# Kernel tuning notes

Hardware: AMD Instinct MI355X
Metric: run time of the kernel (lower is better)

## Reference

```python
import jax, jax.numpy as jnp
import numpy as np

N, E, G = 50000, 400000, 2048
H, C = 4, 64            # heads, hidden per head
IN, ED, TASKS = 29, 6, 12
HC = H * C


def setup_inputs() -> dict:
    key = jax.random.key(0)
    ks = jax.random.split(key, 20)
    s = 0.1
    f32 = jnp.float32
    inp = {
        'x': jax.random.normal(ks[0], (N, IN), f32),
        'edge_index': jax.random.randint(ks[1], (2, E), 0, N),
        'edge_attr': jax.random.normal(ks[2], (E, ED), f32),
        'batch': jnp.sort(jax.random.randint(ks[3], (N,), 0, G)),
        # layer 1 (in=29 -> H*C=256)
        'W1': jax.random.normal(ks[4], (IN, HC), f32) * s,
        'as1': jax.random.normal(ks[5], (1, H, C), f32) * s,
        'ad1': jax.random.normal(ks[6], (1, H, C), f32) * s,
        'We1': jax.random.normal(ks[7], (ED, HC), f32) * s,
        'ae1': jax.random.normal(ks[8], (1, H, C), f32) * s,
        'b1': jnp.zeros((HC,), f32),
        # layer 2 (in=256 -> 256)
        'W2': jax.random.normal(ks[9], (HC, HC), f32) * s,
        'as2': jax.random.normal(ks[10], (1, H, C), f32) * s,
        'ad2': jax.random.normal(ks[11], (1, H, C), f32) * s,
        'We2': jax.random.normal(ks[12], (ED, HC), f32) * s,
        'ae2': jax.random.normal(ks[13], (1, H, C), f32) * s,
        'b2': jnp.zeros((HC,), f32),
        # readout linear (256 -> 12)
        'Wl': jax.random.normal(ks[14], (HC, TASKS), f32) * s,
        'bl': jnp.zeros((TASKS,), f32),
    }
    return inp


def _gat_conv(x, src, dst, eattr, W, a_src, a_dst, We, a_e, b):
    """PyG GATConv, concat=True, leaky_relu slope 0.2, self-loops already appended."""
    h = (x @ W).reshape(N, H, C)                      # [N,H,C]
    al_s = jnp.sum(h * a_src, axis=-1)                # [N,H]
    al_d = jnp.sum(h * a_dst, axis=-1)                # [N,H]
    he = (eattr @ We).reshape(-1, H, C)               # [Etot,H,C]
    al_e = jnp.sum(he * a_e, axis=-1)                 # [Etot,H]
    alpha = al_s[src] + al_d[dst] + al_e              # [Etot,H]
    alpha = jax.nn.leaky_relu(alpha, negative_slope=0.2)
    # segment softmax over incoming edges of each dst node
    amax = jax.ops.segment_max(alpha, dst, num_segments=N)
    ex = jnp.exp(alpha - amax[dst])
    denom = jax.ops.segment_sum(ex, dst, num_segments=N)
    alpha = ex / (denom[dst] + 1e-16)
    msg = h[src] * alpha[:, :, None]                  # [Etot,H,C]
    out = jax.ops.segment_sum(msg, dst, num_segments=N)
    return out.reshape(N, HC) + b


def reference(x, edge_index, edge_attr, batch,
              W1, as1, ad1, We1, ae1, b1,
              W2, as2, ad2, We2, ae2, b2, Wl, bl):
    # add self-loops with edge_attr fill = mean over existing edges (PyG default)
    loop = jnp.arange(N)
    src = jnp.concatenate([edge_index[0], loop])
    dst = jnp.concatenate([edge_index[1], loop])
    mean_e = jnp.mean(edge_attr, axis=0, keepdims=True)
    eattr = jnp.concatenate([edge_attr, jnp.broadcast_to(mean_e, (N, ED))], axis=0)

    h = _gat_conv(x, src, dst, eattr, W1, as1, ad1, We1, ae1, b1)
    h = jax.nn.relu(h)
    h = _gat_conv(h, src, dst, eattr, W2, as2, ad2, We2, ae2, b2)
    h = jax.nn.relu(h)

    # global mean pool over graphs
    sums = jax.ops.segment_sum(h, batch, num_segments=G)      # [G,HC]
    cnt = jax.ops.segment_sum(jnp.ones((N,), h.dtype), batch, num_segments=G)
    pooled = sums / jnp.maximum(cnt, 1.0)[:, None]
    return pooled @ Wl + bl
```

## Files before the change

kernel.cpp:

```cpp
#include <hip/hip_runtime.h>
#include <math.h>

static constexpr int NN = 50000;
static constexpr int EE = 400000;
static constexpr int GG = 2048;
static constexpr int TASKS = 12;

typedef __attribute__((ext_vector_type(8))) short short8;
typedef __attribute__((ext_vector_type(4))) float floatx4;

__device__ __forceinline__ unsigned short f2bf(float f) {
  unsigned u = __float_as_uint(f);
  u = u + 0x7fffu + ((u >> 16) & 1u);
  return (unsigned short)(u >> 16);
}
__device__ __forceinline__ float bflo(unsigned u) { return __uint_as_float(u << 16); }
__device__ __forceinline__ float bfhi(unsigned u) { return __uint_as_float(u & 0xffff0000u); }

static constexpr int NBDEG = (EE + 255) / 256;
static constexpr int NBMEAN = 256;
static constexpr int NBX = (NN * 4 + 255) / 256;
static constexpr int NW1 = 32;
static constexpr int NW2 = 256;
__global__ void k_pre(const int* __restrict__ dst, const float* __restrict__ ea,
                      const float* __restrict__ x, const float* __restrict__ W1,
                      const float* __restrict__ W2, int* __restrict__ deg,
                      float* __restrict__ msum, unsigned short* __restrict__ xb,
                      unsigned short* __restrict__ w1t, unsigned short* __restrict__ w2t) {
  const int b = blockIdx.x;
  const int t = threadIdx.x;
  if (b < NBDEG) {
    int e = b * 256 + t;
    if (e < EE) atomicAdd(&deg[dst[e]], 1);
  } else if (b < NBDEG + NBMEAN) {
    float s[6] = {0, 0, 0, 0, 0, 0};
    for (int e = (b - NBDEG) * 256 + t; e < EE; e += NBMEAN * 256) {
#pragma unroll
      for (int d = 0; d < 6; d++) s[d] += ea[(size_t)e * 6 + d];
    }
    __shared__ float ls[6];
    if (t < 6) ls[t] = 0.f;
    __syncthreads();
#pragma unroll
    for (int d = 0; d < 6; d++) atomicAdd(&ls[d], s[d]);
    __syncthreads();
    if (t < 6) atomicAdd(&msum[t], ls[t]);
  } else if (b < NBDEG + NBMEAN + NBX) {
    int i = (b - NBDEG - NBMEAN) * 256 + t;
    if (i < NN * 4) {
      int n = i >> 2, seg = i & 3;
      unsigned short v[8];
#pragma unroll
      for (int j = 0; j < 8; j++) {
        int k = seg * 8 + j;
        v[j] = (k < 29) ? f2bf(x[(size_t)n * 29 + k]) : (unsigned short)0;
      }
      *(short8*)(xb + (size_t)n * 32 + seg * 8) = *(short8*)v;
    }
  } else if (b < NBDEG + NBMEAN + NBX + NW1) {
    int i = (b - NBDEG - NBMEAN - NBX) * 256 + t;
    int row = i >> 5, k = i & 31;
    unsigned short v = (k < 29) ? f2bf(W1[(size_t)k * 256 + row]) : (unsigned short)0;
    w1t[((row >> 4) * 4 + (k >> 3)) * 128 + (row & 15) * 8 + (k & 7)] = v;
  } else {
    int i = (b - NBDEG - NBMEAN - NBX - NW1) * 256 + t;
    int row = i >> 8, k = i & 255;
    w2t[((row >> 4) * 32 + (k >> 3)) * 128 + (row & 15) * 8 + (k & 7)] = f2bf(W2[(size_t)k * 256 + row]);
  }
}

static constexpr int NBS = (NN + 255) / 256;

__global__ void k_scan1(const int* __restrict__ deg, int* __restrict__ rowptr,
                        int* __restrict__ bsums, const float* __restrict__ We1,
                        const float* __restrict__ ae1, const float* __restrict__ We2,
                        const float* __restrict__ ae2, const float* __restrict__ msum,
                        float* __restrict__ p1, float* __restrict__ p2) {
  const int t = threadIdx.x;
  if (blockIdx.x >= NBS) {
    const int layer = blockIdx.x - NBS;
    const float* We = layer ? We2 : We1;
    const float* ae = layer ? ae2 : ae1;
    float* params = layer ? p2 : p1;
    __shared__ float vsh[24];
    if (t < 24) {
      int d = t >> 2, h = t & 3;
      float s = 0.f;
      for (int c = 0; c < 64; c++) s += We[d * 256 + h * 64 + c] * ae[h * 64 + c];
      vsh[t] = s;
      params[t] = s;
    }
    __syncthreads();
    if (t < 4) {
      float s = 0.f;
      const float invE = 1.0f / (float)EE;
#pragma unroll
      for (int d = 0; d < 6; d++) s += (msum[d] * invE) * vsh[d * 4 + t];
      params[24 + t] = s;
    }
    return;
  }
  __shared__ int sh[256];
  int i = blockIdx.x * 256 + t;
  int v = (i < NN) ? deg[i] : 0;
  sh[t] = v;
  __syncthreads();
  for (int off = 1; off < 256; off <<= 1) {
    int tv = (t >= off) ? sh[t - off] : 0;
    __syncthreads();
    sh[t] += tv;
    __syncthreads();
  }
  if (i < NN) rowptr[i] = sh[t] - v;
  if (t == 255) bsums[blockIdx.x] = sh[255];
}

__global__ void k_scan23(int* __restrict__ rowptr, const int* __restrict__ bsums, int nb) {
  __shared__ int sh[256];
  const int t = threadIdx.x;
  sh[t] = (t < nb) ? bsums[t] : 0;
  __syncthreads();
  for (int off = 1; off < 256; off <<= 1) {
    int tv = (t >= off) ? sh[t - off] : 0;
    __syncthreads();
    sh[t] += tv;
    __syncthreads();
  }
  const int add = (blockIdx.x == 0) ? 0 : sh[blockIdx.x - 1];
  int i = blockIdx.x * 256 + t;
  if (i < NN) rowptr[i] += add;
  if (i == 0) rowptr[NN] = EE;
}

template <int KP>
__device__ __forceinline__ void gemm_body(
    int bx, const unsigned short* __restrict__ A, const unsigned short* __restrict__ Bt,
    const float* __restrict__ a_s, const float* __restrict__ a_d,
    unsigned short* __restrict__ Y, float* __restrict__ als, float* __restrict__ ald, int M) {
  __shared__ __align__(16) unsigned short Ash[64 * KP];
  const int tid = threadIdx.x;
  const int lane = tid & 63;
  const int w = tid >> 6;
  const int l15 = lane & 15;
  const int quad = lane >> 4;
  const int row0 = bx * 64;

  constexpr int STEPS = (64 * KP * 2) / (256 * 16);
  {
    const char* Ab = (const char*)(A + (size_t)row0 * KP);
    uint4 stg[STEPS];
#pragma unroll
    for (int s = 0; s < STEPS; s++) stg[s] = *(const uint4*)(Ab + s * 4096 + tid * 16);
#pragma unroll
    for (int s = 0; s < STEPS; s++) {
      int o = s * 4096 + tid * 16;
      int row = o / (KP * 2);
      *(uint4*)((char*)Ash + (o ^ ((row & 7) << 4))) = stg[s];
    }
  }

  floatx4 acc[4][4];
#pragma unroll
  for (int i = 0; i < 4; i++)
#pragma unroll
    for (int j = 0; j < 4; j++) acc[i][j] = {0.f, 0.f, 0.f, 0.f};

  const unsigned short* pb[4];
#pragma unroll
  for (int j = 0; j < 4; j++)
    pb[j] = Bt + (size_t)((w * 4 + j) * (KP / 8) + quad) * 128 + l15 * 8;

  constexpr int NPH = KP / 32;
  short8 bfr[3][4];
#pragma unroll
  for (int j = 0; j < 4; j++) bfr[0][j] = *(const short8*)pb[j];
  if (NPH > 1) {
#pragma unroll
    for (int j = 0; j < 4; j++) {
      pb[j] += 512;
      bfr[1][j] = *(const short8*)pb[j];
    }
  }

  __syncthreads();

  auto ldA = [&](int ph, short8 (&dst)[4]) {
#pragma unroll
    for (int i = 0; i < 4; i++) {
      int lin = (i * 16 + l15) * (KP * 2) + ph * 64 + quad * 16;
      dst[i] = *(const short8*)((const char*)Ash + (lin ^ ((l15 & 7) << 4)));
    }
  };
  short8 af[2][4];
  ldA(0, af[0]);

#pragma unroll
  for (int ph = 0; ph < NPH; ph++) {
    if (ph + 2 < NPH) {
#pragma unroll
      for (int j = 0; j < 4; j++) {
        pb[j] += 512;
        bfr[(ph + 2) % 3][j] = *(const short8*)pb[j];
      }
    }
    if (ph + 1 < NPH) ldA(ph + 1, af[(ph + 1) & 1]);
#pragma unroll
    for (int i = 0; i < 4; i++)
#pragma unroll
      for (int j = 0; j < 4; j++)
        acc[i][j] = __builtin_amdgcn_mfma_f32_16x16x32_bf16(af[ph & 1][i], bfr[ph % 3][j], acc[i][j], 0, 0, 0);
  }
  float asc[4], adc[4];
#pragma unroll
  for (int j = 0; j < 4; j++) {
    asc[j] = a_s[w * 64 + j * 16 + l15];
    adc[j] = a_d[w * 64 + j * 16 + l15];
  }
#pragma unroll
  for (int i = 0; i < 4; i++) {
#pragma unroll
    for (int r = 0; r < 4; r++) {
      const int row = row0 + i * 16 + quad * 4 + r;
      unsigned ub[4];
      float hv[4];
#pragma unroll
      for (int j = 0; j < 4; j++) {
        ub[j] = f2bf(acc[i][j][r]);
        hv[j] = __uint_as_float(ub[j] << 16);
      }
      if (row < M) {
#pragma unroll
        for (int j = 0; j < 4; j++) Y[(size_t)row * 256 + w * 64 + j * 16 + l15] = (unsigned short)ub[j];
      }
      float ps = hv[0] * asc[0] + hv[1] * asc[1] + hv[2] * asc[2] + hv[3] * asc[3];
      float pd = hv[0] * adc[0] + hv[1] * adc[1] + hv[2] * adc[2] + hv[3] * adc[3];
#pragma unroll
      for (int off = 1; off < 16; off <<= 1) {
        ps += __shfl_xor(ps, off, 64);
        pd += __shfl_xor(pd, off, 64);
      }
      if (l15 == 0 && row < M) {
        als[row * 4 + w] = ps;
        ald[row * 4 + w] = pd;
      }
    }
  }
}

static constexpr int GB = (NN + 63) / 64;

__global__ __launch_bounds__(256, 2) void k_scatgemm1(
    const int* __restrict__ ei, const int* __restrict__ rowptr, int* __restrict__ cursor,
    int2* __restrict__ cse,
    const unsigned short* __restrict__ xb, const unsigned short* __restrict__ w1t,
    const float* __restrict__ as1, const float* __restrict__ ad1,
    unsigned short* __restrict__ hb, float* __restrict__ als, float* __restrict__ ald) {
  const int b = blockIdx.x;
  const int t = threadIdx.x;
  if (b < NBDEG) {
    int e = b * 256 + t;
    if (e >= EE) return;
    int s = ei[e];
    int d = ei[EE + e];
    int p = atomicAdd(&cursor[d], 1);
    int slot = rowptr[d] + p;
    cse[slot] = make_int2(s, e);
  } else {
    gemm_body<32>(b - NBDEG, xb, w1t, as1, ad1, hb, als, ald, NN);
  }
}

__global__ __launch_bounds__(256, 2) void k_gemm2(
    const unsigned short* __restrict__ A, const unsigned short* __restrict__ Bt,
    const float* __restrict__ a_s, const float* __restrict__ a_d,
    unsigned short* __restrict__ Y, float* __restrict__ als, float* __restrict__ ald) {
  gemm_body<256>(blockIdx.x, A, Bt, a_s, a_d, Y, als, ald, NN);
}

__global__ void k_edc(const int2* __restrict__ cse, const float* __restrict__ ea,
                      const float* __restrict__ p1, const float* __restrict__ p2,
                      float* __restrict__ ed1, float* __restrict__ ed2) {
  int slot = blockIdx.x * 256 + threadIdx.x;
  if (slot >= EE) return;
  int e = cse[slot].y;
  const float* ep = ea + (size_t)e * 6;
  float2 e0 = *(const float2*)ep;
  float2 e1 = *(const float2*)(ep + 2);
  float2 e2 = *(const float2*)(ep + 4);
  float c1[4], c2[4];
#pragma unroll
  for (int h = 0; h < 4; h++) {
    c1[h] = e0.x * p1[0 * 4 + h] + e0.y * p1[1 * 4 + h] + e1.x * p1[2 * 4 + h] +
            e1.y * p1[3 * 4 + h] + e2.x * p1[4 * 4 + h] + e2.y * p1[5 * 4 + h];
    c2[h] = e0.x * p2[0 * 4 + h] + e0.y * p2[1 * 4 + h] + e1.x * p2[2 * 4 + h] +
            e1.y * p2[3 * 4 + h] + e2.x * p2[4 * 4 + h] + e2.y * p2[5 * 4 + h];
  }
  *(float4*)(ed1 + (size_t)slot * 4) = make_float4(c1[0], c1[1], c1[2], c1[3]);
  *(float4*)(ed2 + (size_t)slot * 4) = make_float4(c2[0], c2[1], c2[2], c2[3]);
}

__device__ __forceinline__ float leaky02(float x) { return x > 0.f ? x : 0.2f * x; }

__global__ __launch_bounds__(256) void k_agg(
    const unsigned short* __restrict__ hinb, const float* __restrict__ als,
    const float* __restrict__ ald, const int* __restrict__ rowptr, const int2* __restrict__ cse,
    const float* __restrict__ edc, const float* __restrict__ params, const float* __restrict__ bias,
    unsigned short* __restrict__ houtb) {
  const int lane = threadIdx.x & 63;
  const int n = blockIdx.x * 4 + (threadIdx.x >> 6);
  if (n >= NN) return;
  const int half = lane >> 5;
  const int sl = lane & 31;
  const int head = sl >> 3;

  const float aldn = ald[n * 4 + head];
  float acc[8];
  float ssum;
  {
    float slg = leaky02(als[n * 4 + head] + aldn + params[24 + head]);
    float exs = __expf(slg);
    float wgt = (half == 0) ? exs : 0.f;
    ssum = wgt;
    uint4 uv = *(const uint4*)(hinb + (size_t)n * 256 + sl * 8);
    acc[0] = bflo(uv.x) * wgt;
    acc[1] = bfhi(uv.x) * wgt;
    acc[2] = bflo(uv.y) * wgt;
    acc[3] = bfhi(uv.y) * wgt;
    acc[4] = bflo(uv.z) * wgt;
    acc[5] = bfhi(uv.z) * wgt;
    acc[6] = bflo(uv.w) * wgt;
    acc[7] = bfhi(uv.w) * wgt;
  }
  const int end = rowptr[n + 1];
  int s = rowptr[n] + half;
  while (s < end) {
    int sid[4];
    float edv[4];
#pragma unroll
    for (int k = 0; k < 4; k++) {
      const int q = s + 2 * k;
      const bool v = q < end;
      const int idx = v ? q : end - 1;
      sid[k] = cse[idx].x;
      edv[k] = v ? edc[(size_t)idx * 4 + head] : 0.f;
    }
    float alv[4];
#pragma unroll
    for (int k = 0; k < 4; k++) alv[k] = als[(size_t)sid[k] * 4 + head];
    uint4 r[4];
#pragma unroll
    for (int k = 0; k < 4; k++) {
      r[k] = make_uint4(0u, 0u, 0u, 0u);
      if (s + 2 * k < end) r[k] = *(const uint4*)(hinb + (size_t)sid[k] * 256 + sl * 8);
    }
#pragma unroll
    for (int k = 0; k < 4; k++) {
      const float ex = (s + 2 * k < end) ? __expf(leaky02(alv[k] + aldn + edv[k])) : 0.f;
      acc[0] += bflo(r[k].x) * ex;
      acc[1] += bfhi(r[k].x) * ex;
      acc[2] += bflo(r[k].y) * ex;
      acc[3] += bfhi(r[k].y) * ex;
      acc[4] += bflo(r[k].z) * ex;
      acc[5] += bfhi(r[k].z) * ex;
      acc[6] += bflo(r[k].w) * ex;
      acc[7] += bfhi(r[k].w) * ex;
      ssum += ex;
    }
    s += 8;
  }
#pragma unroll
  for (int j = 0; j < 8; j++) acc[j] += __shfl_xor(acc[j], 32, 64);
  ssum += __shfl_xor(ssum, 32, 64);
  if (half == 0) {
    const float inv = 1.f / (ssum + 1e-16f);
    float4 b0 = *(const float4*)(bias + sl * 8);
    float4 b1 = *(const float4*)(bias + sl * 8 + 4);
    const float bb[8] = {b0.x, b0.y, b0.z, b0.w, b1.x, b1.y, b1.z, b1.w};
    uint p[4];
#pragma unroll
    for (int j = 0; j < 4; j++) {
      float e0 = fmaxf(acc[2 * j] * inv + bb[2 * j], 0.f);
      float e1 = fmaxf(acc[2 * j + 1] * inv + bb[2 * j + 1], 0.f);
      p[j] = (uint)f2bf(e0) | ((uint)f2bf(e1) << 16);
    }
    *(uint4*)(houtb + (size_t)n * 256 + sl * 8) = make_uint4(p[0], p[1], p[2], p[3]);
  }
}

__global__ __launch_bounds__(256) void k_pool(const unsigned short* __restrict__ hb,
                                              const int* __restrict__ batch,
                                              const float* __restrict__ Wl,
                                              const float* __restrict__ bl,
                                              float* __restrict__ out) {
  int g = blockIdx.x;
  int t = threadIdx.x;
  int lo = 0, hi = NN;
  while (lo < hi) {
    int mid = (lo + hi) >> 1;
    if (batch[mid] < g) lo = mid + 1; else hi = mid;
  }
  int start = lo;
  hi = NN;
  while (lo < hi) {
    int mid = (lo + hi) >> 1;
    if (batch[mid] < g + 1) lo = mid + 1; else hi = mid;
  }
  int end = lo;
  const int mid2 = start + ((end - start) >> 1);
  __shared__ float sp[256], sq[256];
  {
    const int c = t & 127;
    const int hseg = t >> 7;
    const int a = hseg ? mid2 : start;
    const int b = hseg ? end : mid2;
    float s0 = 0.f, s1 = 0.f;
    for (int n2 = a; n2 < b; n2++) {
      uint u = ((const uint*)(hb + (size_t)n2 * 256))[c];
      s0 += bflo(u);
      s1 += bfhi(u);
    }
    float* dst = hseg ? sq : sp;
    dst[2 * c] = s0;
    dst[2 * c + 1] = s1;
  }
  __syncthreads();
  if (t < TASKS) {
    float invc = 1.f / fmaxf((float)(end - start), 1.f);
    float o = bl[t];
    for (int c = 0; c < 256; c++) o += (sp[c] + sq[c]) * invc * Wl[c * 12 + t];
    out[(size_t)g * 12 + t] = o;
  }
}

extern "C" void kernel_launch(void* const* d_in, const int* in_sizes, int n_in,
                              void* d_out, int out_size, void* d_ws, size_t ws_size,
                              hipStream_t stream) {
  const float* x = (const float*)d_in[0];
  const int* ei = (const int*)d_in[1];
  const float* ea = (const float*)d_in[2];
  const int* batch = (const int*)d_in[3];
  const float* W1 = (const float*)d_in[4];
  const float* as1 = (const float*)d_in[5];
  const float* ad1 = (const float*)d_in[6];
  const float* We1 = (const float*)d_in[7];
  const float* ae1 = (const float*)d_in[8];
  const float* b1 = (const float*)d_in[9];
  const float* W2 = (const float*)d_in[10];
  const float* as2 = (const float*)d_in[11];
  const float* ad2 = (const float*)d_in[12];
  const float* We2 = (const float*)d_in[13];
  const float* ae2 = (const float*)d_in[14];
  const float* b2 = (const float*)d_in[15];
  const float* Wl = (const float*)d_in[16];
  const float* bl = (const float*)d_in[17];
  float* out = (float*)d_out;

  char* ws = (char*)d_ws;
  size_t off = 0;
  auto take = [&](size_t bytes) -> char* {
    char* p = ws + off;
    off = (off + bytes + 255) & ~(size_t)255;
    return p;
  };
  float* msum = (float*)take(8 * 4);
  int* deg = (int*)take((size_t)NN * 4);
  int* cursor = (int*)take((size_t)NN * 4);
  size_t zero_end = off;
  int* rowptr = (int*)take((size_t)(NN + 1) * 4);
  int* bsums = (int*)take(256 * 4);
  int2* cse = (int2*)take((size_t)EE * 8);
  float* ed1 = (float*)take((size_t)EE * 4 * 4);
  float* ed2 = (float*)take((size_t)EE * 4 * 4);
  float* p1 = (float*)take(32 * 4);
  float* p2 = (float*)take(32 * 4);
  float* als = (float*)take((size_t)NN * 4 * 4);
  float* ald = (float*)take((size_t)NN * 4 * 4);
  unsigned short* hb = (unsigned short*)take((size_t)NN * 256 * 2);
  unsigned short* ab = (unsigned short*)take((size_t)NN * 256 * 2);
  unsigned short* xb = (unsigned short*)take((size_t)NN * 32 * 2);
  unsigned short* w1t = (unsigned short*)take((size_t)256 * 32 * 2);
  unsigned short* w2t = (unsigned short*)take((size_t)256 * 256 * 2);
  (void)ws_size;

  hipMemsetAsync(ws, 0, zero_end, stream);

  k_pre<<<NBDEG + NBMEAN + NBX + NW1 + NW2, 256, 0, stream>>>(ei + EE, ea, x, W1, W2,
                                                              deg, msum, xb, w1t, w2t);
  k_scan1<<<NBS + 2, 256, 0, stream>>>(deg, rowptr, bsums, We1, ae1, We2, ae2, msum, p1, p2);
  k_scan23<<<NBS, 256, 0, stream>>>(rowptr, bsums, NBS);

  k_scatgemm1<<<NBDEG + GB, 256, 0, stream>>>(ei, rowptr, cursor, cse,
                                              xb, w1t, as1, ad1, hb, als, ald);

  k_edc<<<NBDEG, 256, 0, stream>>>(cse, ea, p1, p2, ed1, ed2);

  k_agg<<<NN / 4, 256, 0, stream>>>(hb, als, ald, rowptr, cse, ed1, p1, b1, ab);

  k_gemm2<<<GB, 256, 0, stream>>>(ab, w2t, as2, ad2, hb, als, ald);
  k_agg<<<NN / 4, 256, 0, stream>>>(hb, als, ald, rowptr, cse, ed2, p2, b2, ab);

  k_pool<<<GG, 256, 0, stream>>>(ab, batch, Wl, bl, out);
}
```

Baseline: 289.7 us.

## Fuse edge-coefficient computation into CSR scatter with packed 64-byte edge records

The separate k_edc kernel is removed: the scatter step now computes the per-edge attention contributions for both layers and writes them, together with the source and edge ids, into one 64-byte record per CSR slot. The aggregation kernels read the source id and edge term from that record, selected by an offset. This drops one launch and one pass over the CSR array, and gives each edge's data one cache line. The cost is more bytes written and read per edge (64 instead of 24), with padding. The GEMM A-tile load also clamps its addresses so the last tile cannot read past the end of the input.

```diff
diff --git a/kernel.cpp b/kernel.cpp
--- a/kernel.cpp
+++ b/kernel.cpp
@@ -147,10 +147,14 @@
 
   constexpr int STEPS = (64 * KP * 2) / (256 * 16);
   {
-    const char* Ab = (const char*)(A + (size_t)row0 * KP);
+    const size_t limit = (size_t)M * (KP * 2) - 16;
     uint4 stg[STEPS];
 #pragma unroll
-    for (int s = 0; s < STEPS; s++) stg[s] = *(const uint4*)(Ab + s * 4096 + tid * 16);
+    for (int s = 0; s < STEPS; s++) {
+      size_t og = (size_t)row0 * (KP * 2) + s * 4096 + tid * 16;
+      if (og > limit) og = limit;
+      stg[s] = *(const uint4*)((const char*)A + og);
+    }
 #pragma unroll
     for (int s = 0; s < STEPS; s++) {
       int o = s * 4096 + tid * 16;
@@ -251,7 +255,8 @@
 
 __global__ __launch_bounds__(256, 2) void k_scatgemm1(
     const int* __restrict__ ei, const int* __restrict__ rowptr, int* __restrict__ cursor,
-    int2* __restrict__ cse,
+    float* __restrict__ rec, const float* __restrict__ ea,
+    const float* __restrict__ p1, const float* __restrict__ p2,
     const unsigned short* __restrict__ xb, const unsigned short* __restrict__ w1t,
     const float* __restrict__ as1, const float* __restrict__ ad1,
     unsigned short* __restrict__ hb, float* __restrict__ als, float* __restrict__ ald) {
@@ -264,7 +269,23 @@
     int d = ei[EE + e];
     int p = atomicAdd(&cursor[d], 1);
     int slot = rowptr[d] + p;
-    cse[slot] = make_int2(s, e);
+    const float* ep = ea + (size_t)e * 6;
+    float2 e0 = *(const float2*)ep;
+    float2 e1 = *(const float2*)(ep + 2);
+    float2 e2 = *(const float2*)(ep + 4);
+    float c1[4], c2[4];
+#pragma unroll
+    for (int h = 0; h < 4; h++) {
+      c1[h] = e0.x * p1[0 * 4 + h] + e0.y * p1[1 * 4 + h] + e1.x * p1[2 * 4 + h] +
+              e1.y * p1[3 * 4 + h] + e2.x * p1[4 * 4 + h] + e2.y * p1[5 * 4 + h];
+      c2[h] = e0.x * p2[0 * 4 + h] + e0.y * p2[1 * 4 + h] + e1.x * p2[2 * 4 + h] +
+              e1.y * p2[3 * 4 + h] + e2.x * p2[4 * 4 + h] + e2.y * p2[5 * 4 + h];
+    }
+    float* rp = rec + (size_t)slot * 16;
+    *(float4*)rp = make_float4(__int_as_float(s), __int_as_float(e), 0.f, 0.f);
+    *(float4*)(rp + 4) = make_float4(c1[0], c1[1], c1[2], c1[3]);
+    *(float4*)(rp + 8) = make_float4(c2[0], c2[1], c2[2], c2[3]);
+    *(float4*)(rp + 12) = make_float4(0.f, 0.f, 0.f, 0.f);
   } else {
     gemm_body<32>(b - NBDEG, xb, w1t, as1, ad1, hb, als, ald, NN);
   }
@@ -277,34 +298,12 @@
   gemm_body<256>(blockIdx.x, A, Bt, a_s, a_d, Y, als, ald, NN);
 }
 
-__global__ void k_edc(const int2* __restrict__ cse, const float* __restrict__ ea,
-                      const float* __restrict__ p1, const float* __restrict__ p2,
-                      float* __restrict__ ed1, float* __restrict__ ed2) {
-  int slot = blockIdx.x * 256 + threadIdx.x;
-  if (slot >= EE) return;
-  int e = cse[slot].y;
-  const float* ep = ea + (size_t)e * 6;
-  float2 e0 = *(const float2*)ep;
-  float2 e1 = *(const float2*)(ep + 2);
-  float2 e2 = *(const float2*)(ep + 4);
-  float c1[4], c2[4];
-#pragma unroll
-  for (int h = 0; h < 4; h++) {
-    c1[h] = e0.x * p1[0 * 4 + h] + e0.y * p1[1 * 4 + h] + e1.x * p1[2 * 4 + h] +
-            e1.y * p1[3 * 4 + h] + e2.x * p1[4 * 4 + h] + e2.y * p1[5 * 4 + h];
-    c2[h] = e0.x * p2[0 * 4 + h] + e0.y * p2[1 * 4 + h] + e1.x * p2[2 * 4 + h] +
-            e1.y * p2[3 * 4 + h] + e2.x * p2[4 * 4 + h] + e2.y * p2[5 * 4 + h];
-  }
-  *(float4*)(ed1 + (size_t)slot * 4) = make_float4(c1[0], c1[1], c1[2], c1[3]);
-  *(float4*)(ed2 + (size_t)slot * 4) = make_float4(c2[0], c2[1], c2[2], c2[3]);
-}
-
 __device__ __forceinline__ float leaky02(float x) { return x > 0.f ? x : 0.2f * x; }
 
 __global__ __launch_bounds__(256) void k_agg(
     const unsigned short* __restrict__ hinb, const float* __restrict__ als,
-    const float* __restrict__ ald, const int* __restrict__ rowptr, const int2* __restrict__ cse,
-    const float* __restrict__ edc, const float* __restrict__ params, const float* __restrict__ bias,
+    const float* __restrict__ ald, const int* __restrict__ rowptr, const float* __restrict__ rec,
+    int edoff, const float* __restrict__ params, const float* __restrict__ bias,
     unsigned short* __restrict__ houtb) {
   const int lane = threadIdx.x & 63;
   const int n = blockIdx.x * 4 + (threadIdx.x >> 6);
@@ -341,8 +340,9 @@
       const int q = s + 2 * k;
       const bool v = q < end;
       const int idx = v ? q : end - 1;
-      sid[k] = cse[idx].x;
-      edv[k] = v ? edc[(size_t)idx * 4 + head] : 0.f;
+      const float* rp = rec + (size_t)idx * 16;
+      sid[k] = __float_as_int(rp[0]);
+      edv[k] = v ? rp[edoff + head] : 0.f;
     }
     float alv[4];
 #pragma unroll
@@ -468,9 +468,7 @@
   size_t zero_end = off;
   int* rowptr = (int*)take((size_t)(NN + 1) * 4);
   int* bsums = (int*)take(256 * 4);
-  int2* cse = (int2*)take((size_t)EE * 8);
-  float* ed1 = (float*)take((size_t)EE * 4 * 4);
-  float* ed2 = (float*)take((size_t)EE * 4 * 4);
+  float* rec = (float*)take((size_t)EE * 64);
   float* p1 = (float*)take(32 * 4);
   float* p2 = (float*)take(32 * 4);
   float* als = (float*)take((size_t)NN * 4 * 4);
@@ -489,15 +487,13 @@
   k_scan1<<<NBS + 2, 256, 0, stream>>>(deg, rowptr, bsums, We1, ae1, We2, ae2, msum, p1, p2);
   k_scan23<<<NBS, 256, 0, stream>>>(rowptr, bsums, NBS);
 
-  k_scatgemm1<<<NBDEG + GB, 256, 0, stream>>>(ei, rowptr, cursor, cse,
+  k_scatgemm1<<<NBDEG + GB, 256, 0, stream>>>(ei, rowptr, cursor, rec, ea, p1, p2,
                                               xb, w1t, as1, ad1, hb, als, ald);
 
-  k_edc<<<NBDEG, 256, 0, stream>>>(cse, ea, p1, p2, ed1, ed2);
-
-  k_agg<<<NN / 4, 256, 0, stream>>>(hb, als, ald, rowptr, cse, ed1, p1, b1, ab);
+  k_agg<<<NN / 4, 256, 0, stream>>>(hb, als, ald, rowptr, rec, 4, p1, b1, ab);
 
   k_gemm2<<<GB, 256, 0, stream>>>(ab, w2t, as2, ad2, hb, als, ald);
-  k_agg<<<NN / 4, 256, 0, stream>>>(hb, als, ald, rowptr, cse, ed2, p2, b2, ab);
+  k_agg<<<NN / 4, 256, 0, stream>>>(hb, als, ald, rowptr, rec, 8, p2, b2, ab);
 
   k_pool<<<GG, 256, 0, stream>>>(ab, batch, Wl, bl, out);
 }
```

Measured after the change: 286.2 us. About the same (-1.2%).
